# Kernel optimization log

Hardware: AMD Instinct MI355X
Metric: run time of the kernel (lower is better)

The kernel has to match this reference:

```python
import jax, jax.numpy as jnp
import numpy as np

B, NUM, D = 8192, 8, 4096

def setup_inputs() -> dict:
    key = jax.random.key(0)
    k1, k2, k3 = jax.random.split(key, 3)
    x = jax.random.normal(k1, (B, D), dtype=jnp.float32)
    experts = jax.random.normal(k2, (B, NUM, D), dtype=jnp.float32)
    W = jax.random.normal(k3, (NUM, D), dtype=jnp.float32) * (1.0 / np.sqrt(D))
    return {"x": x, "experts": experts, "W": W}

def reference(x, experts, W):
    # gate logits: fused version of num separate Linear(input_dim,1) layers
    logits = jnp.einsum('bd,nd->bn', x, W)          # [B, num]
    weights = jax.nn.softmax(logits, axis=1)          # [B, num]
    # weighted combine of expert outputs (bmm([B,1,num],[B,num,d]).squeeze())
    return jnp.einsum('bn,bnd->bd', weights, experts) # [B, d]
```

## Files before the change

kernel.cpp:

```cpp
#include <hip/hip_runtime.h>
#include <math.h>

#define NUM_E 8
#define DIM 4096
#define THREADS 256
#define WAVES 4
#define VEC_ITERS (DIM / (THREADS * 4))
#define ROWS 2

typedef float f32x4 __attribute__((ext_vector_type(4)));

__device__ __forceinline__ f32x4 nt_load4(const float* p) {
    return __builtin_nontemporal_load(reinterpret_cast<const f32x4*>(p));
}
__device__ __forceinline__ void nt_store4(float* p, f32x4 v) {
    __builtin_nontemporal_store(v, reinterpret_cast<f32x4*>(p));
}

__device__ __forceinline__ void reduce_softmax(float p[NUM_E],
                                               float (*red)[NUM_E],
                                               int lane, int wave,
                                               float wgt[NUM_E],
                                               bool pre_barrier)
{
#pragma unroll
    for (int n = 0; n < NUM_E; ++n) {
#pragma unroll
        for (int off = 32; off > 0; off >>= 1)
            p[n] += __shfl_down(p[n], off, 64);
    }
    if (pre_barrier) __syncthreads();
    if (lane == 0) {
#pragma unroll
        for (int n = 0; n < NUM_E; ++n) red[wave][n] = p[n];
    }
    __syncthreads();
#pragma unroll
    for (int n = 0; n < NUM_E; ++n)
        wgt[n] = red[0][n] + red[1][n] + red[2][n] + red[3][n];
    float m = wgt[0];
#pragma unroll
    for (int n = 1; n < NUM_E; ++n) m = fmaxf(m, wgt[n]);
    float sum = 0.0f;
#pragma unroll
    for (int n = 0; n < NUM_E; ++n) {
        wgt[n] = __expf(wgt[n] - m);
        sum += wgt[n];
    }
    const float inv = 1.0f / sum;
#pragma unroll
    for (int n = 0; n < NUM_E; ++n) wgt[n] *= inv;
}

__global__ __launch_bounds__(THREADS) void gate_pipelined_kernel(
    const float* __restrict__ x,
    const float* __restrict__ experts,
    const float* __restrict__ W,
    float* __restrict__ out)
{
    const int b0   = blockIdx.x * ROWS;
    const int t    = threadIdx.x;
    const int lane = t & 63;
    const int wave = t >> 6;

    __shared__ float red[WAVES][NUM_E];

    const float* __restrict__ x0 = x + (size_t)b0 * DIM;
    float p[NUM_E];
#pragma unroll
    for (int n = 0; n < NUM_E; ++n) p[n] = 0.0f;
#pragma unroll
    for (int i = 0; i < VEC_ITERS; ++i) {
        const int d = (i * THREADS + t) * 4;
        const f32x4 xv = nt_load4(x0 + d);
#pragma unroll
        for (int n = 0; n < NUM_E; ++n) {
            const f32x4 wv = *reinterpret_cast<const f32x4*>(W + n * DIM + d);
            p[n] += xv.x * wv.x + xv.y * wv.y + xv.z * wv.z + xv.w * wv.w;
        }
    }
    float wgt0[NUM_E];
    reduce_softmax(p, red, lane, wave, wgt0, false);

    const float* __restrict__ e0 = experts + (size_t)b0 * NUM_E * DIM;
    float* __restrict__ o0 = out + (size_t)b0 * DIM;
    const float* __restrict__ x1 = x + (size_t)(b0 + 1) * DIM;

    f32x4 xv[VEC_ITERS];
#pragma unroll
    for (int i = 0; i < VEC_ITERS; ++i)
        xv[i] = nt_load4(x1 + (i * THREADS + t) * 4);

    float p1[NUM_E];
#pragma unroll
    for (int n = 0; n < NUM_E; ++n) p1[n] = 0.0f;

    f32x4 acc[VEC_ITERS];
#pragma unroll
    for (int i = 0; i < VEC_ITERS; ++i) acc[i] = (f32x4)(0.0f);

#pragma unroll
    for (int n = 0; n < NUM_E; ++n) {
        const float wn = wgt0[n];
#pragma unroll
        for (int i = 0; i < VEC_ITERS; ++i) {
            const int d = (i * THREADS + t) * 4;
            const f32x4 ev = nt_load4(e0 + (size_t)n * DIM + d);
            acc[i].x += wn * ev.x;
            acc[i].y += wn * ev.y;
            acc[i].z += wn * ev.z;
            acc[i].w += wn * ev.w;
            const f32x4 wv = *reinterpret_cast<const f32x4*>(W + n * DIM + d);
            p1[n] += xv[i].x * wv.x + xv[i].y * wv.y + xv[i].z * wv.z + xv[i].w * wv.w;
        }
    }
#pragma unroll
    for (int i = 0; i < VEC_ITERS; ++i)
        nt_store4(o0 + (i * THREADS + t) * 4, acc[i]);

    float wgt1[NUM_E];
    reduce_softmax(p1, red, lane, wave, wgt1, true);

    const float* __restrict__ e1 = experts + (size_t)(b0 + 1) * NUM_E * DIM;
    float* __restrict__ o1 = out + (size_t)(b0 + 1) * DIM;

#pragma unroll
    for (int i = 0; i < VEC_ITERS; ++i) acc[i] = (f32x4)(0.0f);

#pragma unroll
    for (int n = 0; n < NUM_E; ++n) {
        const float wn = wgt1[n];
#pragma unroll
        for (int i = 0; i < VEC_ITERS; ++i) {
            const int d = (i * THREADS + t) * 4;
            const f32x4 ev = nt_load4(e1 + (size_t)n * DIM + d);
            acc[i].x += wn * ev.x;
            acc[i].y += wn * ev.y;
            acc[i].z += wn * ev.z;
            acc[i].w += wn * ev.w;
        }
    }
#pragma unroll
    for (int i = 0; i < VEC_ITERS; ++i)
        nt_store4(o1 + (i * THREADS + t) * 4, acc[i]);
}

extern "C" void kernel_launch(void* const* d_in, const int* in_sizes, int n_in,
                              void* d_out, int out_size, void* d_ws, size_t ws_size,
                              hipStream_t stream) {
    const float* x       = (const float*)d_in[0];
    const float* experts = (const float*)d_in[1];
    const float* W       = (const float*)d_in[2];
    float* out           = (float*)d_out;

    const int B = in_sizes[0] / DIM;

    gate_pipelined_kernel<<<B / ROWS, THREADS, 0, stream>>>(x, experts, W, out);
}
```

Measured before the change: 233.5 us.

## Compute both rows' gate logits together before combining experts

Rewrites the two-row kernel so the gate dot products for both rows are computed in one pass over W, followed by a single shared-memory reduction, one barrier and both softmaxes. After that, the two expert-combine passes run back to back. This removes the earlier software pipeline that overlapped row 1's gate computation with row 0's expert streaming, and it drops one barrier. It also adds a launch-bounds occupancy hint of 8 blocks, which may constrain register allocation.

Result: slower. 297.2 us (+27.3%).

```diff
diff --git a/kernel.cpp b/kernel.cpp
--- a/kernel.cpp
+++ b/kernel.cpp
@@ -17,42 +17,7 @@
     __builtin_nontemporal_store(v, reinterpret_cast<f32x4*>(p));
 }
 
-__device__ __forceinline__ void reduce_softmax(float p[NUM_E],
-                                               float (*red)[NUM_E],
-                                               int lane, int wave,
-                                               float wgt[NUM_E],
-                                               bool pre_barrier)
-{
-#pragma unroll
-    for (int n = 0; n < NUM_E; ++n) {
-#pragma unroll
-        for (int off = 32; off > 0; off >>= 1)
-            p[n] += __shfl_down(p[n], off, 64);
-    }
-    if (pre_barrier) __syncthreads();
-    if (lane == 0) {
-#pragma unroll
-        for (int n = 0; n < NUM_E; ++n) red[wave][n] = p[n];
-    }
-    __syncthreads();
-#pragma unroll
-    for (int n = 0; n < NUM_E; ++n)
-        wgt[n] = red[0][n] + red[1][n] + red[2][n] + red[3][n];
-    float m = wgt[0];
-#pragma unroll
-    for (int n = 1; n < NUM_E; ++n) m = fmaxf(m, wgt[n]);
-    float sum = 0.0f;
-#pragma unroll
-    for (int n = 0; n < NUM_E; ++n) {
-        wgt[n] = __expf(wgt[n] - m);
-        sum += wgt[n];
-    }
-    const float inv = 1.0f / sum;
-#pragma unroll
-    for (int n = 0; n < NUM_E; ++n) wgt[n] *= inv;
-}
-
-__global__ __launch_bounds__(THREADS) void gate_pipelined_kernel(
+__global__ __launch_bounds__(THREADS, 8) void gate_dual_kernel(
     const float* __restrict__ x,
     const float* __restrict__ experts,
     const float* __restrict__ W,
@@ -63,86 +28,114 @@
     const int lane = t & 63;
     const int wave = t >> 6;
 
-    __shared__ float red[WAVES][NUM_E];
+    __shared__ float red[ROWS][WAVES][NUM_E];
 
     const float* __restrict__ x0 = x + (size_t)b0 * DIM;
-    float p[NUM_E];
+    const float* __restrict__ x1 = x + (size_t)(b0 + 1) * DIM;
+
+    float p0[NUM_E], p1[NUM_E];
 #pragma unroll
-    for (int n = 0; n < NUM_E; ++n) p[n] = 0.0f;
+    for (int n = 0; n < NUM_E; ++n) { p0[n] = 0.0f; p1[n] = 0.0f; }
+
 #pragma unroll
     for (int i = 0; i < VEC_ITERS; ++i) {
         const int d = (i * THREADS + t) * 4;
-        const f32x4 xv = nt_load4(x0 + d);
+        const f32x4 x0v = nt_load4(x0 + d);
+        const f32x4 x1v = nt_load4(x1 + d);
 #pragma unroll
         for (int n = 0; n < NUM_E; ++n) {
             const f32x4 wv = *reinterpret_cast<const f32x4*>(W + n * DIM + d);
-            p[n] += xv.x * wv.x + xv.y * wv.y + xv.z * wv.z + xv.w * wv.w;
+            p0[n] += x0v.x * wv.x + x0v.y * wv.y + x0v.z * wv.z + x0v.w * wv.w;
+            p1[n] += x1v.x * wv.x + x1v.y * wv.y + x1v.z * wv.z + x1v.w * wv.w;
         }
     }
-    float wgt0[NUM_E];
-    reduce_softmax(p, red, lane, wave, wgt0, false);
-
-    const float* __restrict__ e0 = experts + (size_t)b0 * NUM_E * DIM;
-    float* __restrict__ o0 = out + (size_t)b0 * DIM;
-    const float* __restrict__ x1 = x + (size_t)(b0 + 1) * DIM;
-
-    f32x4 xv[VEC_ITERS];
-#pragma unroll
-    for (int i = 0; i < VEC_ITERS; ++i)
-        xv[i] = nt_load4(x1 + (i * THREADS + t) * 4);
-
-    float p1[NUM_E];
-#pragma unroll
-    for (int n = 0; n < NUM_E; ++n) p1[n] = 0.0f;
-
-    f32x4 acc[VEC_ITERS];
-#pragma unroll
-    for (int i = 0; i < VEC_ITERS; ++i) acc[i] = (f32x4)(0.0f);
 
 #pragma unroll
     for (int n = 0; n < NUM_E; ++n) {
-        const float wn = wgt0[n];
 #pragma unroll
-        for (int i = 0; i < VEC_ITERS; ++i) {
-            const int d = (i * THREADS + t) * 4;
-            const f32x4 ev = nt_load4(e0 + (size_t)n * DIM + d);
-            acc[i].x += wn * ev.x;
-            acc[i].y += wn * ev.y;
-            acc[i].z += wn * ev.z;
-            acc[i].w += wn * ev.w;
-            const f32x4 wv = *reinterpret_cast<const f32x4*>(W + n * DIM + d);
-            p1[n] += xv[i].x * wv.x + xv[i].y * wv.y + xv[i].z * wv.z + xv[i].w * wv.w;
+        for (int off = 32; off > 0; off >>= 1) {
+            p0[n] += __shfl_down(p0[n], off, 64);
+            p1[n] += __shfl_down(p1[n], off, 64);
         }
     }
+    if (lane == 0) {
 #pragma unroll
-    for (int i = 0; i < VEC_ITERS; ++i)
-        nt_store4(o0 + (i * THREADS + t) * 4, acc[i]);
-
-    float wgt1[NUM_E];
-    reduce_softmax(p1, red, lane, wave, wgt1, true);
-
-    const float* __restrict__ e1 = experts + (size_t)(b0 + 1) * NUM_E * DIM;
-    float* __restrict__ o1 = out + (size_t)(b0 + 1) * DIM;
-
-#pragma unroll
-    for (int i = 0; i < VEC_ITERS; ++i) acc[i] = (f32x4)(0.0f);
-
-#pragma unroll
-    for (int n = 0; n < NUM_E; ++n) {
-        const float wn = wgt1[n];
-#pragma unroll
-        for (int i = 0; i < VEC_ITERS; ++i) {
-            const int d = (i * THREADS + t) * 4;
-            const f32x4 ev = nt_load4(e1 + (size_t)n * DIM + d);
-            acc[i].x += wn * ev.x;
-            acc[i].y += wn * ev.y;
-            acc[i].z += wn * ev.z;
-            acc[i].w += wn * ev.w;
+        for (int n = 0; n < NUM_E; ++n) {
+            red[0][wave][n] = p0[n];
+            red[1][wave][n] = p1[n];
         }
     }
+    __syncthreads();
+
+    float wgt0[NUM_E], wgt1[NUM_E];
+    {
 #pragma unroll
-    for (int i = 0; i < VEC_ITERS; ++i)
-        nt_store4(o1 + (i * THREADS + t) * 4, acc[i]);
+        for (int n = 0; n < NUM_E; ++n) {
+            wgt0[n] = red[0][0][n] + red[0][1][n] + red[0][2][n] + red[0][3][n];
+            wgt1[n] = red[1][0][n] + red[1][1][n] + red[1][2][n] + red[1][3][n];
+        }
+        float m0 = wgt0[0], m1 = wgt1[0];
+#pragma unroll
+        for (int n = 1; n < NUM_E; ++n) {
+            m0 = fmaxf(m0, wgt0[n]);
+            m1 = fmaxf(m1, wgt1[n]);
+        }
+        float s0 = 0.0f, s1 = 0.0f;
+#pragma unroll
+        for (int n = 0; n < NUM_E; ++n) {
+            wgt0[n] = __expf(wgt0[n] - m0); s0 += wgt0[n];
+            wgt1[n] = __expf(wgt1[n] - m1); s1 += wgt1[n];
+        }
+        const float i0 = 1.0f / s0, i1 = 1.0f / s1;
+#pragma unroll
+        for (int n = 0; n < NUM_E; ++n) { wgt0[n] *= i0; wgt1[n] *= i1; }
+    }
+
+    {
+        const float* __restrict__ e0 = experts + (size_t)b0 * NUM_E * DIM;
+        float* __restrict__ o0 = out + (size_t)b0 * DIM;
+        f32x4 acc[VEC_ITERS];
+#pragma unroll
+        for (int i = 0; i < VEC_ITERS; ++i) acc[i] = (f32x4)(0.0f);
+#pragma unroll
+        for (int n = 0; n < NUM_E; ++n) {
+            const float wn = wgt0[n];
+#pragma unroll
+            for (int i = 0; i < VEC_ITERS; ++i) {
+                const f32x4 ev = nt_load4(e0 + (size_t)n * DIM + (i * THREADS + t) * 4);
+                acc[i].x += wn * ev.x;
+                acc[i].y += wn * ev.y;
+                acc[i].z += wn * ev.z;
+                acc[i].w += wn * ev.w;
+            }
+        }
+#pragma unroll
+        for (int i = 0; i < VEC_ITERS; ++i)
+            nt_store4(o0 + (i * THREADS + t) * 4, acc[i]);
+    }
+
+    {
+        const float* __restrict__ e1 = experts + (size_t)(b0 + 1) * NUM_E * DIM;
+        float* __restrict__ o1 = out + (size_t)(b0 + 1) * DIM;
+        f32x4 acc[VEC_ITERS];
+#pragma unroll
+        for (int i = 0; i < VEC_ITERS; ++i) acc[i] = (f32x4)(0.0f);
+#pragma unroll
+        for (int n = 0; n < NUM_E; ++n) {
+            const float wn = wgt1[n];
+#pragma unroll
+            for (int i = 0; i < VEC_ITERS; ++i) {
+                const f32x4 ev = nt_load4(e1 + (size_t)n * DIM + (i * THREADS + t) * 4);
+                acc[i].x += wn * ev.x;
+                acc[i].y += wn * ev.y;
+                acc[i].z += wn * ev.z;
+                acc[i].w += wn * ev.w;
+            }
+        }
+#pragma unroll
+        for (int i = 0; i < VEC_ITERS; ++i)
+            nt_store4(o1 + (i * THREADS + t) * 4, acc[i]);
+    }
 }
 
 extern "C" void kernel_launch(void* const* d_in, const int* in_sizes, int n_in,
@@ -155,5 +148,5 @@
 
     const int B = in_sizes[0] / DIM;
 
-    gate_pipelined_kernel<<<B / ROWS, THREADS, 0, stream>>>(x, experts, W, out);
+    gate_dual_kernel<<<B / ROWS, THREADS, 0, stream>>>(x, experts, W, out);
 }
```
